# Optimization experiments

Hardware: AMD Instinct MI355X
Metric: run time of the kernel (lower is better)

Reference implementation:

```python
import jax, jax.numpy as jnp
import numpy as np
from jax import lax

STRIDE = 2
PAD = 2
K = 5

def conv_transpose3d(x, w, b):
    # x: (N, Cin, D, H, W); w: (Cin, Cout, kD, kH, kW) torch layout
    # Equivalent dense conv: flip kernel spatially, swap in/out, lhs-dilate by stride,
    # pad each side by (K - 1 - PAD).
    w_t = jnp.flip(w, axis=(2, 3, 4)).transpose(1, 0, 2, 3, 4)  # (Cout, Cin, kD, kH, kW)
    p = K - 1 - PAD  # = 2
    y = lax.conv_general_dilated(
        x, w_t,
        window_strides=(1, 1, 1),
        padding=[(p, p)] * 3,
        lhs_dilation=(STRIDE,) * 3,
        dimension_numbers=('NCDHW', 'OIDHW', 'NCDHW'))
    return y + b[None, :, None, None, None]

def maxpool3d(x, k):
    return lax.reduce_window(
        x, -jnp.inf, lax.max,
        window_dimensions=(1, 1, k, k, k),
        window_strides=(1, 1, k, k, k),
        padding='VALID')

def setup_inputs() -> dict:
    key = jax.random.key(0)
    k1, k2, k3 = jax.random.split(key, 3)
    x = jax.random.normal(k1, (16, 32, 16, 32, 32), dtype=jnp.float32)
    weight = jax.random.normal(k2, (32, 64, 5, 5, 5), dtype=jnp.float32) * 0.05
    bias = jax.random.normal(k3, (64,), dtype=jnp.float32) * 0.05
    return {"x": x, "weight": weight, "bias": bias}

def reference(x, weight, bias):
    y = conv_transpose3d(x, weight, bias)      # (16, 64, 31, 63, 63)
    y = maxpool3d(y, 2)                        # (16, 64, 15, 31, 31)
    y = maxpool3d(y, 3)                        # (16, 64, 5, 10, 10)
    return jnp.sum(y, axis=1, keepdims=True)   # (16, 1, 5, 10, 10)
```

## Files before the change

### kernel.cpp

```cpp
#include <hip/hip_runtime.h>

typedef short v8s __attribute__((ext_vector_type(8)));
typedef float v4f __attribute__((ext_vector_type(4)));

#define N_  16
#define CI_ 32
#define CO_ 64
#define DI  16
#define HI  32
#define WI  32
#define NEGINF (-__builtin_inff())

__device__ __forceinline__ unsigned short f2bf(float f) {
    unsigned int u = __float_as_uint(f);
    unsigned int r = (u + 0x7FFFu + ((u >> 16) & 1u)) >> 16;
    return (unsigned short)r;
}

__device__ __forceinline__ void gld16(const void* g, void* l) {
    __builtin_amdgcn_global_load_lds(
        (const __attribute__((address_space(1))) void*)g,
        (__attribute__((address_space(3))) void*)l, 16, 0, 0);
}

__constant__ int O64c[9] = {0, 55296, 92160, 129024, 153600, 190464, 215040, 239616, 256000};

__global__ void prep(const float* __restrict__ x, const float* __restrict__ w,
                     unsigned short* __restrict__ xp, unsigned short* __restrict__ wt,
                     int do_x) {
    if (blockIdx.x < 4488) {
        if (!do_x) return;
        int t = blockIdx.x * 256 + threadIdx.x;
        int pw = t % 33;
        int q1 = t / 33;
        int ph = q1 & 31;
        int q2 = q1 >> 5;
        int pd = q2 % 17;
        int q3 = q2 / 17;
        int cg = q3 & 3;
        int n  = q3 >> 2;
        v8s o;
        if (pd == 0 || ph == 0 || pw == 0) {
            o = (v8s){0, 0, 0, 0, 0, 0, 0, 0};
        } else {
            const float* xb = x + ((((size_t)(n * 32 + cg * 8) * 16 + (pd - 1)) * 32
                                    + (ph - 1)) * 32 + (pw - 1));
            #pragma unroll
            for (int c = 0; c < 8; ++c)
                o[c] = (short)f2bf(xb[(size_t)c * 16384]);
        }
        *(v8s*)(xp + (size_t)t * 8) = o;
    } else {
        int u = (blockIdx.x - 4488) * 256 + threadIdx.x;
        if (u >= 256000) return;
        int r = 0;
        #pragma unroll
        for (int i = 1; i < 8; ++i) r += (u >= O64c[i]);
        const int rd = r >> 2, rh = (r >> 1) & 1, rw = r & 1;
        const int nh = rh ? 2 : 3, nw = rw ? 2 : 3;
        int t2 = u - O64c[r];
        int j   = t2 & 7;
        int l   = (t2 >> 3) & 15;
        int q   = (t2 >> 7) & 3;
        int nt  = (t2 >> 9) & 3;
        int tap = t2 >> 11;
        int co = nt * 16 + l;
        int ci = q * 8 + j;
        int jw = tap % nw;
        int jh = (tap / nw) % nh;
        int jd = tap / (nw * nh);
        int kd = rd + 2 * jd, kh = rh + 2 * jh, kw = rw + 2 * jw;
        wt[u] = f2bf(w[(ci * CO_ + co) * 125 + kd * 25 + kh * 5 + kw]);
    }
}

template<bool PAR>
__device__ __forceinline__ void run_class(
        const unsigned short* __restrict__ xs,
        int laneAB,
        const unsigned short* __restrict__ wcls,
        const int taps, const int nw, const int nh,
        unsigned Bm, bool isQ3, float (&pmax)[4][2])
{
    constexpr int T  = PAR ? 4 : 5;
    constexpr int R0 = PAR ? 288 : 0;
    constexpr int R1 = PAR ? 1440 : 576;
    constexpr int R2 = PAR ? 2016 : 1728;
    constexpr int R3 = PAR ? 3168 : 2880;
    constexpr int R4 = 3456;

    const char* xb = (const char*)xs;

    v4f acc[T][4];
    #pragma unroll
    for (int t = 0; t < T; ++t)
        #pragma unroll
        for (int nt = 0; nt < 4; ++nt)
            acc[t][nt] = (v4f){0.f, 0.f, 0.f, 0.f};

    v8s B0[4], B1[4];
    #pragma unroll
    for (int nt = 0; nt < 4; ++nt) B0[nt] = *(const v8s*)(wcls + nt * 512);

    int aoff = 0, jw = 0, jh = 0;
    auto adv = [&]() {
        aoff += 16; ++jw;
        if (jw == nw) { jw = 0; aoff += 288 - 16 * nw; ++jh;
            if (jh == nh) { jh = 0; aoff += 1440 - 288 * nh; } }
    };
    auto comp = [&](const v8s (&B)[4]) {
        const int va = laneAB - aoff;
        v8s a0 = *(const v8s*)(xb + va + R0);
        v8s a1 = *(const v8s*)(xb + va + R1);
        v8s a2 = *(const v8s*)(xb + va + R2);
        v8s a3 = *(const v8s*)(xb + va + R3);
        v8s a4;
        if (!PAR) a4 = *(const v8s*)(xb + va + R4);
        #pragma unroll
        for (int nt = 0; nt < 4; ++nt) {
            acc[0][nt] = __builtin_amdgcn_mfma_f32_16x16x32_bf16(a0, B[nt], acc[0][nt], 0, 0, 0);
            acc[1][nt] = __builtin_amdgcn_mfma_f32_16x16x32_bf16(a1, B[nt], acc[1][nt], 0, 0, 0);
            acc[2][nt] = __builtin_amdgcn_mfma_f32_16x16x32_bf16(a2, B[nt], acc[2][nt], 0, 0, 0);
            acc[3][nt] = __builtin_amdgcn_mfma_f32_16x16x32_bf16(a3, B[nt], acc[3][nt], 0, 0, 0);
            if (!PAR)
                acc[4][nt] = __builtin_amdgcn_mfma_f32_16x16x32_bf16(a4, B[nt], acc[4][nt], 0, 0, 0);
        }
    };

    int s = 0;
    while (s + 2 <= taps) {
        #pragma unroll
        for (int nt = 0; nt < 4; ++nt)
            B1[nt] = *(const v8s*)(wcls + ((s + 1) * 4 + nt) * 512);
        comp(B0); adv();
        if (s + 2 < taps) {
            #pragma unroll
            for (int nt = 0; nt < 4; ++nt)
                B0[nt] = *(const v8s*)(wcls + ((s + 2) * 4 + nt) * 512);
        }
        comp(B1); adv();
        s += 2;
    }
    if (s < taps) comp(B0);

    #pragma unroll
    for (int nt = 0; nt < 4; ++nt) {
        #pragma unroll
        for (int reg = 0; reg < 4; ++reg) {
            float v = acc[0][nt][reg];
            #pragma unroll
            for (int t = 1; t < T; ++t) v = fmaxf(v, acc[t][nt][reg]);
            if (reg == 3) v = isQ3 ? NEGINF : v;
            const bool bB = (Bm >> reg) & 1u;
            pmax[nt][0] = fmaxf(pmax[nt][0], bB ? NEGINF : v);
            pmax[nt][1] = fmaxf(pmax[nt][1], bB ? v : NEGINF);
        }
    }
}

template<bool PRE>
__global__ __launch_bounds__(512, 3)
void fused_main(const float* __restrict__ x, const unsigned short* __restrict__ xp,
                const unsigned short* __restrict__ wt,
                const float* __restrict__ bias, float* __restrict__ out) {
    __shared__ __align__(16) char smem[28800];
    unsigned short* xs = (unsigned short*)smem;
    float* P = (float*)smem;
    float* Y = (float*)(smem + 20736);

    const int b = blockIdx.x;
    const int whalf = b & 1;
    const int hj = (b >> 1) % 10;
    const int dj = (b / 20) % 5;
    const int n  = b / 100;

    const int lane = threadIdx.x & 63;
    const int wv   = threadIdx.x >> 6;

    if (PRE) {
        const int t = threadIdx.x;
        #pragma unroll
        for (int i = 0; i < 4; ++i) {
            int c = i * 512 + t;
            if (c < 1800) {
                int row = c / 18;
                int iwc = c - row * 18;
                int cg  = row / 25;
                int rr  = row - cg * 25;
                int idl = rr / 5;
                int ihl = rr - idl * 5;
                size_t goff = ((((size_t)((n * 4 + cg) * 17 + 3 * dj + idl)) * 32
                                + 3 * hj + ihl) * 33 + 15 * whalf + iwc) * 8;
                gld16(xp + goff, smem + i * 8192 + wv * 1024);
            }
        }
    } else {
        const int id0 = 3 * dj - 1, ih0 = 3 * hj - 1, iwb = 15 * whalf - 1;
        const float* xn = x + (size_t)n * (CI_ * DI * HI * WI);
        for (int e = threadIdx.x; e < 14400; e += 512) {
            int ci   = e / 450;
            int rem  = e - ci * 450;
            int idp  = rem / 90;
            int rem2 = rem - idp * 90;
            int ihp  = rem2 / 18;
            int iwp  = rem2 - ihp * 18;
            int id = id0 + idp, ih = ih0 + ihp, iw = iwb + iwp;
            float v = 0.f;
            if (id >= 0 && ih >= 0 && iw >= 0)
                v = xn[((ci * DI + id) * HI + ih) * WI + iw];
            xs[(ci >> 3) * 3600 + idp * 720 + ihp * 144 + iwp * 8 + (ci & 7)] = f2bf(v);
        }
    }
    __syncthreads();

    const int l = lane & 15, q = lane >> 4;
    const int pi = wv >> 1;
    const int wp = wv & 1;

    const int laneAB = q * 7200 + (l + 2) * 16 + 3456;

    static constexpr int PT[4][2] = {{0, 7}, {1, 3}, {2, 5}, {4, 6}};
    static constexpr int tapsT[8] = {27, 18, 18, 12, 18, 12, 12, 8};
    static constexpr int O64[8]   = {0, 55296, 92160, 129024, 153600, 190464, 215040, 239616};
    static constexpr int nwT[8]   = {3, 2, 3, 2, 3, 2, 3, 2};
    static constexpr int nhT[8]   = {3, 3, 2, 2, 3, 3, 2, 2};

    float pmax[4][2];
    #pragma unroll
    for (int nt = 0; nt < 4; ++nt) { pmax[nt][0] = NEGINF; pmax[nt][1] = NEGINF; }

    const unsigned Bm = (0x0EC8u >> (q << 2)) & 0xFu;
    const bool isQ3 = (q == 3);

    #pragma unroll 1
    for (int c4 = 0; c4 < 2; ++c4) {
        const int r = PT[pi][c4];
        const int taps = tapsT[r], nw = nwT[r], nh = nhT[r];
        const unsigned short* wcls = wt + O64[r] + lane * 8;
        if ((wp + c4) & 1)
            run_class<true >(xs, laneAB, wcls, taps, nw, nh, Bm, isQ3, pmax);
        else
            run_class<false>(xs, laneAB, wcls, taps, nw, nh, Bm, isQ3, pmax);
    }

    __syncthreads();
    {
        int base = ((wv * 4 + q) * 16 + l) * 9;
        #pragma unroll
        for (int nt = 0; nt < 4; ++nt) {
            P[base + nt * 2 + 0] = pmax[nt][0];
            P[base + nt * 2 + 1] = pmax[nt][1];
        }
    }
    __syncthreads();

    static constexpr int wjAt[4] = {0, 1, 2, 4};
    static constexpr int wjBt[4] = {1, 2, 3, 5};
    if (threadIdx.x < 320) {
        int oi = threadIdx.x;
        int co = oi / 5;
        int wjl = oi - co * 5;
        int lc = co & 15, ntc = co >> 4;
        float v = NEGINF;
        #pragma unroll
        for (int w = 0; w < 8; ++w) {
            #pragma unroll
            for (int qq = 0; qq < 4; ++qq) {
                const float* pp = &P[((w * 4 + qq) * 16 + lc) * 9 + ntc * 2];
                if (wjAt[qq] == wjl) v = fmaxf(v, pp[0]);
                if (wjBt[qq] == wjl) v = fmaxf(v, pp[1]);
            }
        }
        Y[co * 5 + wjl] = v + bias[co];
    }
    __syncthreads();

    if (threadIdx.x < 5) {
        float s = 0.f;
        #pragma unroll
        for (int co = 0; co < 64; ++co) s += Y[co * 5 + threadIdx.x];
        out[((n * 5 + dj) * 10 + hj) * 10 + whalf * 5 + threadIdx.x] = s;
    }
}

extern "C" void kernel_launch(void* const* d_in, const int* in_sizes, int n_in,
                              void* d_out, int out_size, void* d_ws, size_t ws_size,
                              hipStream_t stream) {
    const float* x    = (const float*)d_in[0];
    const float* w    = (const float*)d_in[1];
    const float* bias = (const float*)d_in[2];
    float*       out  = (float*)d_out;
    unsigned short* wt = (unsigned short*)d_ws;
    unsigned short* xp = (unsigned short*)((char*)d_ws + 512512);
    const size_t XP_NEED = 512512 + 18382848;
    const int do_x = (ws_size >= XP_NEED) ? 1 : 0;

    prep<<<dim3(5488), 256, 0, stream>>>(x, w, xp, wt, do_x);
    if (do_x)
        fused_main<true ><<<dim3(1600), 512, 0, stream>>>(x, xp, wt, bias, out);
    else
        fused_main<false><<<dim3(1600), 512, 0, stream>>>(x, xp, wt, bias, out);
}
```

Baseline: 202.0 us.

## Template-unroll tap loops per class and tile the input repack through LDS

After: 248.0 us. 1.23x slower.

```diff
diff --git a/kernel.cpp b/kernel.cpp
--- a/kernel.cpp
+++ b/kernel.cpp
@@ -28,30 +28,32 @@
 __global__ void prep(const float* __restrict__ x, const float* __restrict__ w,
                      unsigned short* __restrict__ xp, unsigned short* __restrict__ wt,
                      int do_x) {
-    if (blockIdx.x < 4488) {
+    if (blockIdx.x < 1088) {
         if (!do_x) return;
-        int t = blockIdx.x * 256 + threadIdx.x;
-        int pw = t % 33;
-        int q1 = t / 33;
-        int ph = q1 & 31;
-        int q2 = q1 >> 5;
-        int pd = q2 % 17;
-        int q3 = q2 / 17;
-        int cg = q3 & 3;
-        int n  = q3 >> 2;
-        v8s o;
-        if (pd == 0 || ph == 0 || pw == 0) {
-            o = (v8s){0, 0, 0, 0, 0, 0, 0, 0};
-        } else {
-            const float* xb = x + ((((size_t)(n * 32 + cg * 8) * 16 + (pd - 1)) * 32
-                                    + (ph - 1)) * 32 + (pw - 1));
+        __shared__ __align__(16) unsigned short tl[8192];
+        const int bi = blockIdx.x;
+        const int pd = bi % 17;
+        const int cg = (bi / 17) & 3;
+        const int n  = bi / 68;
+        if (pd > 0) {
+            const int c = threadIdx.x >> 5;
+            const int ww = threadIdx.x & 31;
+            const float* xc = x + (((size_t)(n * 32 + cg * 8 + c) * 16 + (pd - 1)) * 32) * 32;
             #pragma unroll
-            for (int c = 0; c < 8; ++c)
-                o[c] = (short)f2bf(xb[(size_t)c * 16384]);
-        }
-        *(v8s*)(xp + (size_t)t * 8) = o;
+            for (int h = 0; h < 32; ++h)
+                tl[(h * 32 + ww) * 8 + c] = f2bf(xc[h * 32 + ww]);
+        }
+        __syncthreads();
+        unsigned short* xpo = xp + (size_t)bi * 8448;
+        for (int o = threadIdx.x; o < 1056; o += 256) {
+            int ph = o / 33, pw = o - ph * 33;
+            v8s v;
+            if (pd == 0 || ph == 0 || pw == 0) v = (v8s){0, 0, 0, 0, 0, 0, 0, 0};
+            else v = *(const v8s*)&tl[((ph - 1) * 32 + pw - 1) * 8];
+            *(v8s*)(xpo + o * 8) = v;
+        }
     } else {
-        int u = (blockIdx.x - 4488) * 256 + threadIdx.x;
+        int u = (blockIdx.x - 1088) * 256 + threadIdx.x;
         if (u >= 256000) return;
         int r = 0;
         #pragma unroll
@@ -74,12 +76,10 @@
     }
 }
 
-template<bool PAR>
+template<int ND, int NH, int NW, bool PAR>
 __device__ __forceinline__ void run_class(
-        const unsigned short* __restrict__ xs,
-        int laneAB,
-        const unsigned short* __restrict__ wcls,
-        const int taps, const int nw, const int nh,
+        const char* __restrict__ xq,
+        const v8s* __restrict__ wb,
         unsigned Bm, bool isQ3, float (&pmax)[4][2])
 {
     constexpr int T  = PAR ? 4 : 5;
@@ -89,8 +89,6 @@
     constexpr int R3 = PAR ? 3168 : 2880;
     constexpr int R4 = 3456;
 
-    const char* xb = (const char*)xs;
-
     v4f acc[T][4];
     #pragma unroll
     for (int t = 0; t < T; ++t)
@@ -98,24 +96,23 @@
         for (int nt = 0; nt < 4; ++nt)
             acc[t][nt] = (v4f){0.f, 0.f, 0.f, 0.f};
 
-    v8s B0[4], B1[4];
-    #pragma unroll
-    for (int nt = 0; nt < 4; ++nt) B0[nt] = *(const v8s*)(wcls + nt * 512);
-
-    int aoff = 0, jw = 0, jh = 0;
-    auto adv = [&]() {
-        aoff += 16; ++jw;
-        if (jw == nw) { jw = 0; aoff += 288 - 16 * nw; ++jh;
-            if (jh == nh) { jh = 0; aoff += 1440 - 288 * nh; } }
-    };
-    auto comp = [&](const v8s (&B)[4]) {
-        const int va = laneAB - aoff;
-        v8s a0 = *(const v8s*)(xb + va + R0);
-        v8s a1 = *(const v8s*)(xb + va + R1);
-        v8s a2 = *(const v8s*)(xb + va + R2);
-        v8s a3 = *(const v8s*)(xb + va + R3);
+    #pragma unroll
+    for (int jd = 0; jd < ND; ++jd)
+    #pragma unroll
+    for (int jh = 0; jh < NH; ++jh)
+    #pragma unroll
+    for (int jw = 0; jw < NW; ++jw) {
+        const int s  = (jd * NH + jh) * NW + jw;
+        const int ao = 3488 - (1440 * jd + 288 * jh + 16 * jw);
+        v8s B[4];
+        #pragma unroll
+        for (int nt = 0; nt < 4; ++nt) B[nt] = wb[(s * 4 + nt) * 64];
+        v8s a0 = *(const v8s*)(xq + (ao + R0));
+        v8s a1 = *(const v8s*)(xq + (ao + R1));
+        v8s a2 = *(const v8s*)(xq + (ao + R2));
+        v8s a3 = *(const v8s*)(xq + (ao + R3));
         v8s a4;
-        if (!PAR) a4 = *(const v8s*)(xb + va + R4);
+        if (!PAR) a4 = *(const v8s*)(xq + (ao + R4));
         #pragma unroll
         for (int nt = 0; nt < 4; ++nt) {
             acc[0][nt] = __builtin_amdgcn_mfma_f32_16x16x32_bf16(a0, B[nt], acc[0][nt], 0, 0, 0);
@@ -125,23 +122,7 @@
             if (!PAR)
                 acc[4][nt] = __builtin_amdgcn_mfma_f32_16x16x32_bf16(a4, B[nt], acc[4][nt], 0, 0, 0);
         }
-    };
-
-    int s = 0;
-    while (s + 2 <= taps) {
-        #pragma unroll
-        for (int nt = 0; nt < 4; ++nt)
-            B1[nt] = *(const v8s*)(wcls + ((s + 1) * 4 + nt) * 512);
-        comp(B0); adv();
-        if (s + 2 < taps) {
-            #pragma unroll
-            for (int nt = 0; nt < 4; ++nt)
-                B0[nt] = *(const v8s*)(wcls + ((s + 2) * 4 + nt) * 512);
-        }
-        comp(B1); adv();
-        s += 2;
-    }
-    if (s < taps) comp(B0);
+    }
 
     #pragma unroll
     for (int nt = 0; nt < 4; ++nt) {
@@ -159,14 +140,14 @@
 }
 
 template<bool PRE>
-__global__ __launch_bounds__(512, 3)
+__global__ __launch_bounds__(512, 2)
 void fused_main(const float* __restrict__ x, const unsigned short* __restrict__ xp,
                 const unsigned short* __restrict__ wt,
                 const float* __restrict__ bias, float* __restrict__ out) {
     __shared__ __align__(16) char smem[28800];
     unsigned short* xs = (unsigned short*)smem;
     float* P = (float*)smem;
-    float* Y = (float*)(smem + 20736);
+    float* Y = (float*)(smem + 18432);
 
     const int b = blockIdx.x;
     const int whalf = b & 1;
@@ -218,12 +199,10 @@
     const int wp = wv & 1;
 
     const int laneAB = q * 7200 + (l + 2) * 16 + 3456;
-
+    const char* xq = (const char*)xs + (laneAB - 3488);
+
+    static constexpr int O64[8] = {0, 55296, 92160, 129024, 153600, 190464, 215040, 239616};
     static constexpr int PT[4][2] = {{0, 7}, {1, 3}, {2, 5}, {4, 6}};
-    static constexpr int tapsT[8] = {27, 18, 18, 12, 18, 12, 12, 8};
-    static constexpr int O64[8]   = {0, 55296, 92160, 129024, 153600, 190464, 215040, 239616};
-    static constexpr int nwT[8]   = {3, 2, 3, 2, 3, 2, 3, 2};
-    static constexpr int nhT[8]   = {3, 3, 2, 2, 3, 3, 2, 2};
 
     float pmax[4][2];
     #pragma unroll
@@ -232,15 +211,31 @@
     const unsigned Bm = (0x0EC8u >> (q << 2)) & 0xFu;
     const bool isQ3 = (q == 3);
 
-    #pragma unroll 1
-    for (int c4 = 0; c4 < 2; ++c4) {
-        const int r = PT[pi][c4];
-        const int taps = tapsT[r], nw = nwT[r], nh = nhT[r];
-        const unsigned short* wcls = wt + O64[r] + lane * 8;
-        if ((wp + c4) & 1)
-            run_class<true >(xs, laneAB, wcls, taps, nw, nh, Bm, isQ3, pmax);
-        else
-            run_class<false>(xs, laneAB, wcls, taps, nw, nh, Bm, isQ3, pmax);
+    const v8s* wbA = (const v8s*)(wt + O64[PT[pi][0]]) + lane;
+    const v8s* wbB = (const v8s*)(wt + O64[PT[pi][1]]) + lane;
+
+    if (wp == 0) {
+        switch (pi) {
+        case 0: run_class<3,3,3,false>(xq, wbA, Bm, isQ3, pmax);
+                run_class<2,2,2,true >(xq, wbB, Bm, isQ3, pmax); break;
+        case 1: run_class<3,3,2,false>(xq, wbA, Bm, isQ3, pmax);
+                run_class<3,2,2,true >(xq, wbB, Bm, isQ3, pmax); break;
+        case 2: run_class<3,2,3,false>(xq, wbA, Bm, isQ3, pmax);
+                run_class<2,3,2,true >(xq, wbB, Bm, isQ3, pmax); break;
+        default:run_class<2,3,3,false>(xq, wbA, Bm, isQ3, pmax);
+                run_class<2,2,3,true >(xq, wbB, Bm, isQ3, pmax); break;
+        }
+    } else {
+        switch (pi) {
+        case 0: run_class<3,3,3,true >(xq, wbA, Bm, isQ3, pmax);
+                run_class<2,2,2,false>(xq, wbB, Bm, isQ3, pmax); break;
+        case 1: run_class<3,3,2,true >(xq, wbA, Bm, isQ3, pmax);
+                run_class<3,2,2,false>(xq, wbB, Bm, isQ3, pmax); break;
+        case 2: run_class<3,2,3,true >(xq, wbA, Bm, isQ3, pmax);
+                run_class<2,3,2,false>(xq, wbB, Bm, isQ3, pmax); break;
+        default:run_class<2,3,3,true >(xq, wbA, Bm, isQ3, pmax);
+                run_class<2,2,3,false>(xq, wbB, Bm, isQ3, pmax); break;
+        }
     }
 
     __syncthreads();
@@ -295,7 +290,7 @@
     const size_t XP_NEED = 512512 + 18382848;
     const int do_x = (ws_size >= XP_NEED) ? 1 : 0;
 
-    prep<<<dim3(5488), 256, 0, stream>>>(x, w, xp, wt, do_x);
+    prep<<<dim3(2088), 256, 0, stream>>>(x, w, xp, wt, do_x);
     if (do_x)
         fused_main<true ><<<dim3(1600), 512, 0, stream>>>(x, xp, wt, bias, out);
     else
```
